# Kernel optimization log

Hardware: AMD Instinct MI355X
Metric: run time of the kernel (lower is better)

The kernel has to match this reference:

```python
import jax, jax.numpy as jnp
import numpy as np

N_VALUES = 10
STRIDE = 2

# sign binarization with straight-through estimator (identity gradient)
@jax.custom_vjp
def binarize(x):
    return jnp.sign(x)

def _bin_fwd(x):
    return jnp.sign(x), None

def _bin_bwd(res, g):
    return (g,)

binarize.defvjp(_bin_fwd, _bin_bwd)


def setup_inputs() -> dict:
    key = jax.random.key(0)
    k1, k2, k3, k4 = jax.random.split(key, 4)
    B, C, H = 16, 1, 28
    D = 2048
    x = jax.random.uniform(k1, (B, C, H, H), dtype=jnp.float32)          # float image in [0,1)
    values = jax.random.normal(k2, (N_VALUES, D), dtype=jnp.float32)     # value-vector embedding table
    w = jax.random.normal(k3, (D, D, 5, 5), dtype=jnp.float32) * 0.05    # binary conv weight (OIHW)
    b = jax.random.normal(k4, (D,), dtype=jnp.float32) * 0.01            # conv bias
    return {"x": x, "values": values, "w": w, "b": b}


def reference(x, values, w, b):
    n = values.shape[0]
    # quantize pixel intensities to value-vector indices (truncation, like .long())
    idx = (x[:, 0] * (n - 1)).astype(jnp.int32)            # [B, H, W]
    # embedding lookup of binarized value vectors
    emb = binarize(values)[idx]                            # [B, H, W, D]
    emb = jnp.transpose(emb, (0, 3, 1, 2))                 # [B, D, H, W]
    # binary-weight conv2d, kernel 5, stride 2, no padding
    out = jax.lax.conv_general_dilated(
        emb, binarize(w),
        window_strides=(STRIDE, STRIDE), padding='VALID',
        dimension_numbers=('NCHW', 'OIHW', 'NCHW'))
    out = out + b[None, :, None, None]                     # [B, D, 12, 12]
    return binarize(out)
```

## Files before the change

kernel.cpp:

```cpp
#include <hip/hip_runtime.h>

#define NV    10
#define DD    2048
#define TAPS  25
#define CHUNK 128
#define NCH   (DD / CHUNK)
#define NGRP  (DD / 64)
#define OB    64

typedef __attribute__((address_space(1))) const unsigned int gu32;
typedef __attribute__((address_space(3))) unsigned int lu32;

__device__ __forceinline__ float bsign(float v) {
    return (v > 0.0f) ? 1.0f : ((v < 0.0f) ? -1.0f : 0.0f);
}

__global__ __launch_bounds__(64) void vpack_kernel(
        const float* __restrict__ values,
        unsigned long long* __restrict__ vnz,
        unsigned long long* __restrict__ vng) {
    const int b    = blockIdx.x;
    const int n    = b >> 5;
    const int g    = b & 31;
    const int lane = threadIdx.x;
    float f = values[n * DD + g * 64 + lane];
    unsigned long long nz = __ballot(f != 0.0f);
    unsigned long long ng = __ballot(f < 0.0f);
    if (lane == 0) {
        vnz[n * NGRP + g] = nz;
        vng[n * NGRP + g] = ng;
    }
}

__global__ __launch_bounds__(256) void g_kernel(
        const float* __restrict__ w,
        const unsigned long long* __restrict__ gvnz,
        const unsigned long long* __restrict__ gvng,
        float* __restrict__ G) {
    const int o    = blockIdx.x;
    const int t    = threadIdx.x;
    const int lane = t & 63;
    const int wv   = t >> 6;

    __shared__ float ls_raw[CHUNK * TAPS + 32];
    __shared__ unsigned long long s_wnz[2][TAPS * 2];
    __shared__ unsigned long long s_wng[2][TAPS * 2];
    __shared__ unsigned long long s_vnz[NV * NGRP];
    __shared__ unsigned long long s_vng[NV * NGRP];

    const float* wo = w + (size_t)o * (DD * TAPS);

    #define PACK_CHUNK(bi)                                                        \
    {                                                                             \
        _Pragma("unroll")                                                         \
        for (int i = 0; i < 4; ++i) {                                             \
            const int tk = wv + 4 * i;                                            \
            if (tk < 14) {                                                        \
                const int q  = tk >> 1;                                           \
                const int sb = tk & 1;                                            \
                const int t0 = 4 * q;                                             \
                const int ba = (sb * 64 + lane) * TAPS + t0;                      \
                float a0 = ls_raw[ba + 0];                                        \
                float a1 = ls_raw[ba + 1];                                        \
                float a2 = ls_raw[ba + 2];                                        \
                float a3 = ls_raw[ba + 3];                                        \
                unsigned long long z0 = __ballot(a0 != 0.0f);                     \
                unsigned long long g0 = __ballot(a0 <  0.0f);                     \
                unsigned long long z1 = __ballot(a1 != 0.0f);                     \
                unsigned long long g1 = __ballot(a1 <  0.0f);                     \
                unsigned long long z2 = __ballot(a2 != 0.0f);                     \
                unsigned long long g2 = __ballot(a2 <  0.0f);                     \
                unsigned long long z3 = __ballot(a3 != 0.0f);                     \
                unsigned long long g3 = __ballot(a3 <  0.0f);                     \
                if (lane == 0) {                                                  \
                    s_wnz[bi][(t0 + 0) * 2 + sb] = z0;                            \
                    s_wng[bi][(t0 + 0) * 2 + sb] = g0;                            \
                    if (t0 + 1 < TAPS) {                                          \
                        s_wnz[bi][(t0 + 1) * 2 + sb] = z1;                        \
                        s_wng[bi][(t0 + 1) * 2 + sb] = g1;                        \
                        s_wnz[bi][(t0 + 2) * 2 + sb] = z2;                        \
                        s_wng[bi][(t0 + 2) * 2 + sb] = g2;                        \
                        s_wnz[bi][(t0 + 3) * 2 + sb] = z3;                        \
                        s_wng[bi][(t0 + 3) * 2 + sb] = g3;                        \
                    }                                                             \
                }                                                                 \
            }                                                                     \
        }                                                                         \
    }

    for (int e = t; e < (CHUNK * TAPS) / 4; e += 256) {
        __builtin_amdgcn_global_load_lds((gu32*)(wo + 4 * e),
                                         (lu32*)(ls_raw + 4 * (e - lane)), 16, 0, 0);
    }
    for (int e = t; e < NV * NGRP; e += 256) {
        s_vnz[e] = gvnz[e];
        s_vng[e] = gvng[e];
    }
    __syncthreads();
    PACK_CHUNK(0)
    __syncthreads();

    const int tap = t / NV;
    const int n   = t - tap * NV;
    int acc = 0;

    for (int ch = 1; ch <= NCH; ++ch) {
        if (ch < NCH) {
            const float* src = wo + (size_t)(ch * CHUNK) * TAPS;
            for (int e = t; e < (CHUNK * TAPS) / 4; e += 256) {
                __builtin_amdgcn_global_load_lds((gu32*)(src + 4 * e),
                                                 (lu32*)(ls_raw + 4 * (e - lane)), 16, 0, 0);
            }
        }
        if (t < NV * TAPS) {
            const int pb = (ch - 1) & 1;
            #pragma unroll
            for (int sub = 0; sub < 2; ++sub) {
                unsigned long long wnz = s_wnz[pb][tap * 2 + sub];
                unsigned long long wng = s_wng[pb][tap * 2 + sub];
                unsigned long long vz  = s_vnz[n * NGRP + (ch - 1) * 2 + sub];
                unsigned long long vg  = s_vng[n * NGRP + (ch - 1) * 2 + sub];
                unsigned long long nzb = wnz & vz;
                acc += (int)__popcll(nzb) - 2 * (int)__popcll((wng ^ vg) & nzb);
            }
        }
        if (ch < NCH) {
            __syncthreads();
            PACK_CHUNK(ch & 1)
            __syncthreads();
        }
    }
    #undef PACK_CHUNK

    if (t < NV * TAPS) {
        G[((size_t)(tap * NV + n) << 11) + o] = (float)acc;
    }
}

__global__ __launch_bounds__(256) void out_kernel(
        const float* __restrict__ x,
        const float* __restrict__ G,
        const float* __restrict__ bias,
        float* __restrict__ out) {
    const int b     = blockIdx.x >> 5;
    const int oc    = blockIdx.x & 31;
    const int obase = oc * OB;
    const int t     = threadIdx.x;
    const int lane  = t & 63;
    const int oq    = t >> 6;

    __shared__ float s_G[TAPS * NV * 65];
    __shared__ int   s_idx[28 * 28];
    __shared__ float s_bias[OB];

    for (int e = t; e < TAPS * NV * 16; e += 256) {
        const int r  = e >> 4;
        const int li = (e & 15) << 2;
        const float4 v = *(const float4*)(G + ((size_t)r << 11) + obase + li);
        s_G[r * 65 + li]     = v.x;
        s_G[r * 65 + li + 1] = v.y;
        s_G[r * 65 + li + 2] = v.z;
        s_G[r * 65 + li + 3] = v.w;
    }
    for (int e = t; e < 28 * 28; e += 256) {
        s_idx[e] = (int)(x[b * 784 + e] * 9.0f);
    }
    if (t < OB) s_bias[t] = bias[obase + t];
    __syncthreads();

    for (int grp = 0; grp < 3; ++grp) {
        const int pos = grp * 64 + lane;
        if (pos < 144) {
            const int oh = pos / 12;
            const int ow = pos - oh * 12;
            int rr[25];
            #pragma unroll
            for (int kh = 0; kh < 5; ++kh) {
                const int row = (oh * 2 + kh) * 28 + ow * 2;
                #pragma unroll
                for (int kw = 0; kw < 5; ++kw) {
                    const int nn = s_idx[row + kw];
                    rr[kh * 5 + kw] = (kh * 5 + kw) * 650 + nn * 65;
                }
            }
            for (int ol = oq; ol < OB; ol += 4) {
                float acc = 0.0f;
                #pragma unroll
                for (int tp = 0; tp < TAPS; ++tp) {
                    acc += s_G[rr[tp] + ol];
                }
                out[((size_t)(b * DD + obase + ol)) * 144 + pos] = bsign(acc + s_bias[ol]);
            }
        }
    }
}

extern "C" void kernel_launch(void* const* d_in, const int* in_sizes, int n_in,
                              void* d_out, int out_size, void* d_ws, size_t ws_size,
                              hipStream_t stream) {
    const float* x      = (const float*)d_in[0];
    const float* values = (const float*)d_in[1];
    const float* w      = (const float*)d_in[2];
    const float* bias   = (const float*)d_in[3];
    float* out = (float*)d_out;

    unsigned long long* vnz = (unsigned long long*)d_ws;
    unsigned long long* vng = vnz + NV * NGRP;
    float* G = (float*)((char*)d_ws + 8192);

    hipLaunchKernelGGL(vpack_kernel, dim3(NV * NGRP), dim3(64), 0, stream, values, vnz, vng);
    hipLaunchKernelGGL(g_kernel, dim3(DD), dim3(256), 0, stream, w, vnz, vng, G);
    hipLaunchKernelGGL(out_kernel, dim3(16 * (DD / OB)), dim3(256), 0, stream, x, G, bias, out);
}
```

Measured before the change: 119.6 us.

## Double-buffer weight chunks with async LDS loads and manual waitcnt pipelining

Halves the weight staging chunk to 64 input channels and uses two LDS raw buffers, so the load for chunk ch+2 is issued while chunk ch is being packed. The old single-buffer scheme waited on every chunk load. Waits now use explicit s_waitcnt vmcnt/lgkmcnt with raw s_barrier in place of __syncthreads, which lets global-to-LDS transfers overlap the ballot packing and popcount work. In exchange there are twice as many loop iterations and barriers, and correctness depends on the hand-written vmcnt counts being right.

New measurement: 134.9 us. 1.13x slower.

```diff
diff --git a/kernel.cpp b/kernel.cpp
--- a/kernel.cpp
+++ b/kernel.cpp
@@ -3,7 +3,7 @@
 #define NV    10
 #define DD    2048
 #define TAPS  25
-#define CHUNK 128
+#define CHUNK 64
 #define NCH   (DD / CHUNK)
 #define NGRP  (DD / 64)
 #define OB    64
@@ -32,6 +32,17 @@
     }
 }
 
+__device__ __forceinline__ void stage_chunk(const float* __restrict__ gsrc,
+                                            float* lbase, int lane, int wv) {
+    const int b4 = wv * 100;
+    __builtin_amdgcn_global_load_lds((gu32*)(gsrc + 4 * (b4 + lane)),
+                                     (lu32*)(lbase + 4 * b4), 16, 0, 0);
+    if (lane < 36) {
+        __builtin_amdgcn_global_load_lds((gu32*)(gsrc + 4 * (b4 + 64 + lane)),
+                                         (lu32*)(lbase + 4 * (b4 + 64)), 16, 0, 0);
+    }
+}
+
 __global__ __launch_bounds__(256) void g_kernel(
         const float* __restrict__ w,
         const unsigned long long* __restrict__ gvnz,
@@ -42,9 +53,9 @@
     const int lane = t & 63;
     const int wv   = t >> 6;
 
-    __shared__ float ls_raw[CHUNK * TAPS + 32];
-    __shared__ unsigned long long s_wnz[2][TAPS * 2];
-    __shared__ unsigned long long s_wng[2][TAPS * 2];
+    __shared__ float buf[2][1664];
+    __shared__ unsigned long long s_wnz[2][TAPS];
+    __shared__ unsigned long long s_wng[2][TAPS];
     __shared__ unsigned long long s_vnz[NV * NGRP];
     __shared__ unsigned long long s_vng[NV * NGRP];
 
@@ -52,18 +63,17 @@
 
     #define PACK_CHUNK(bi)                                                        \
     {                                                                             \
+        const float* cbuf_ = buf[bi];                                             \
         _Pragma("unroll")                                                         \
-        for (int i = 0; i < 4; ++i) {                                             \
+        for (int i = 0; i < 2; ++i) {                                             \
             const int tk = wv + 4 * i;                                            \
-            if (tk < 14) {                                                        \
-                const int q  = tk >> 1;                                           \
-                const int sb = tk & 1;                                            \
-                const int t0 = 4 * q;                                             \
-                const int ba = (sb * 64 + lane) * TAPS + t0;                      \
-                float a0 = ls_raw[ba + 0];                                        \
-                float a1 = ls_raw[ba + 1];                                        \
-                float a2 = ls_raw[ba + 2];                                        \
-                float a3 = ls_raw[ba + 3];                                        \
+            if (tk < 7) {                                                         \
+                const int t0 = 4 * tk;                                            \
+                const int ba = lane * TAPS + t0;                                  \
+                float a0 = cbuf_[ba + 0];                                         \
+                float a1 = cbuf_[ba + 1];                                         \
+                float a2 = cbuf_[ba + 2];                                         \
+                float a3 = cbuf_[ba + 3];                                         \
                 unsigned long long z0 = __ballot(a0 != 0.0f);                     \
                 unsigned long long g0 = __ballot(a0 <  0.0f);                     \
                 unsigned long long z1 = __ballot(a1 != 0.0f);                     \
@@ -73,62 +83,64 @@
                 unsigned long long z3 = __ballot(a3 != 0.0f);                     \
                 unsigned long long g3 = __ballot(a3 <  0.0f);                     \
                 if (lane == 0) {                                                  \
-                    s_wnz[bi][(t0 + 0) * 2 + sb] = z0;                            \
-                    s_wng[bi][(t0 + 0) * 2 + sb] = g0;                            \
+                    s_wnz[bi][t0] = z0;  s_wng[bi][t0] = g0;                      \
                     if (t0 + 1 < TAPS) {                                          \
-                        s_wnz[bi][(t0 + 1) * 2 + sb] = z1;                        \
-                        s_wng[bi][(t0 + 1) * 2 + sb] = g1;                        \
-                        s_wnz[bi][(t0 + 2) * 2 + sb] = z2;                        \
-                        s_wng[bi][(t0 + 2) * 2 + sb] = g2;                        \
-                        s_wnz[bi][(t0 + 3) * 2 + sb] = z3;                        \
-                        s_wng[bi][(t0 + 3) * 2 + sb] = g3;                        \
+                        s_wnz[bi][t0 + 1] = z1;  s_wng[bi][t0 + 1] = g1;          \
+                        s_wnz[bi][t0 + 2] = z2;  s_wng[bi][t0 + 2] = g2;          \
+                        s_wnz[bi][t0 + 3] = z3;  s_wng[bi][t0 + 3] = g3;          \
                     }                                                             \
                 }                                                                 \
             }                                                                     \
         }                                                                         \
     }
 
-    for (int e = t; e < (CHUNK * TAPS) / 4; e += 256) {
-        __builtin_amdgcn_global_load_lds((gu32*)(wo + 4 * e),
-                                         (lu32*)(ls_raw + 4 * (e - lane)), 16, 0, 0);
-    }
     for (int e = t; e < NV * NGRP; e += 256) {
         s_vnz[e] = gvnz[e];
         s_vng[e] = gvng[e];
     }
-    __syncthreads();
-    PACK_CHUNK(0)
-    __syncthreads();
+    asm volatile("s_waitcnt vmcnt(0) lgkmcnt(0)" ::: "memory");
+    __builtin_amdgcn_sched_barrier(0);
+    stage_chunk(wo,        buf[0], lane, wv);
+    stage_chunk(wo + 1600, buf[1], lane, wv);
+    asm volatile("s_waitcnt vmcnt(2)" ::: "memory");
+    __builtin_amdgcn_sched_barrier(0);
+    __builtin_amdgcn_s_barrier();
 
     const int tap = t / NV;
     const int n   = t - tap * NV;
     int acc = 0;
 
-    for (int ch = 1; ch <= NCH; ++ch) {
-        if (ch < NCH) {
-            const float* src = wo + (size_t)(ch * CHUNK) * TAPS;
-            for (int e = t; e < (CHUNK * TAPS) / 4; e += 256) {
-                __builtin_amdgcn_global_load_lds((gu32*)(src + 4 * e),
-                                                 (lu32*)(ls_raw + 4 * (e - lane)), 16, 0, 0);
-            }
+    for (int ch = 0; ch < NCH; ++ch) {
+        const int cb = ch & 1;
+        PACK_CHUNK(cb)
+        if (ch > 0 && t < NV * TAPS) {
+            unsigned long long wnz = s_wnz[cb ^ 1][tap];
+            unsigned long long wng = s_wng[cb ^ 1][tap];
+            unsigned long long vz  = s_vnz[n * NGRP + (ch - 1)];
+            unsigned long long vg  = s_vng[n * NGRP + (ch - 1)];
+            unsigned long long nzb = wnz & vz;
+            acc += (int)__popcll(nzb) - 2 * (int)__popcll((wng ^ vg) & nzb);
         }
-        if (t < NV * TAPS) {
-            const int pb = (ch - 1) & 1;
-            #pragma unroll
-            for (int sub = 0; sub < 2; ++sub) {
-                unsigned long long wnz = s_wnz[pb][tap * 2 + sub];
-                unsigned long long wng = s_wng[pb][tap * 2 + sub];
-                unsigned long long vz  = s_vnz[n * NGRP + (ch - 1) * 2 + sub];
-                unsigned long long vg  = s_vng[n * NGRP + (ch - 1) * 2 + sub];
-                unsigned long long nzb = wnz & vz;
-                acc += (int)__popcll(nzb) - 2 * (int)__popcll((wng ^ vg) & nzb);
-            }
+        asm volatile("s_waitcnt lgkmcnt(0)" ::: "memory");
+        __builtin_amdgcn_sched_barrier(0);
+        __builtin_amdgcn_s_barrier();
+        if (ch + 2 < NCH) {
+            stage_chunk(wo + (size_t)(ch + 2) * 1600, buf[cb], lane, wv);
+            asm volatile("s_waitcnt vmcnt(2)" ::: "memory");
+        } else {
+            asm volatile("s_waitcnt vmcnt(0)" ::: "memory");
         }
-        if (ch < NCH) {
-            __syncthreads();
-            PACK_CHUNK(ch & 1)
-            __syncthreads();
-        }
+        __builtin_amdgcn_sched_barrier(0);
+        __builtin_amdgcn_s_barrier();
+    }
+    if (t < NV * TAPS) {
+        const int pb = (NCH - 1) & 1;
+        unsigned long long wnz = s_wnz[pb][tap];
+        unsigned long long wng = s_wng[pb][tap];
+        unsigned long long vz  = s_vnz[n * NGRP + (NCH - 1)];
+        unsigned long long vg  = s_vng[n * NGRP + (NCH - 1)];
+        unsigned long long nzb = wnz & vz;
+        acc += (int)__popcll(nzb) - 2 * (int)__popcll((wng ^ vg) & nzb);
     }
     #undef PACK_CHUNK
 
```
